# Kernel tuning notes

Measured on AMD Instinct MI355X. Metric: run time of the kernel, lower is better.

Reference implementation:

```python
import jax, jax.numpy as jnp
import numpy as np

H = 1024      # hidden_dim
C = 151       # len(obj_classes)
E = 200       # embed_dim (GloVe)
DIN = 2048    # inputs_dim
T = 32        # timesteps
B = 128       # batch size (uniform packed lengths)


def setup_inputs() -> dict:
    key = jax.random.key(0)
    ks = jax.random.split(key, 8)
    sequence_tensor = jax.random.normal(ks[0], (T * B, DIN), dtype=jnp.float32) * 0.1
    labels = jax.random.randint(ks[1], (T * B,), 0, C).astype(jnp.int64)
    embed = jax.random.normal(ks[2], (C + 1, E), dtype=jnp.float32) * 0.1   # obj_embed.weight
    Wi = jax.random.normal(ks[3], (DIN + E, 6 * H), dtype=jnp.float32) * 0.02  # input_linearity
    bi = jnp.zeros((6 * H,), dtype=jnp.float32)
    Ws = jax.random.normal(ks[4], (H, 5 * H), dtype=jnp.float32) * 0.02        # state_linearity
    bs = jnp.zeros((5 * H,), dtype=jnp.float32)
    Wo = jax.random.normal(ks[5], (H, C), dtype=jnp.float32) * 0.02            # out_obj
    bo = jnp.zeros((C,), dtype=jnp.float32)
    return {"sequence_tensor": sequence_tensor, "labels": labels, "embed": embed,
            "Wi": Wi, "bi": bi, "Ws": Ws, "bs": bs, "Wo": Wo, "bo": bo,
            "batch_size": B}


def reference(sequence_tensor, embed, Wi, bi, Ws, bs, Wo, bo, labels, batch_size):
    b = int(batch_size)
    t = sequence_tensor.shape[0] // b
    x = sequence_tensor.reshape(t, b, -1)          # [T, B, DIN] packed timestep-major
    lab = labels.reshape(t, b)                     # [T, B]
    h0 = jnp.zeros((b, H), dtype=sequence_tensor.dtype)
    c0 = jnp.zeros((b, H), dtype=sequence_tensor.dtype)
    e0 = jnp.broadcast_to(embed[0], (b, E))        # 'start' embedding

    def step(carry, inp):
        h, c, pe = carry
        xt, lt = inp
        ti = jnp.concatenate([xt, pe], axis=1)     # [B, DIN+E]
        pi = ti @ Wi + bi                          # [B, 6H]
        ps = h @ Ws + bs                           # [B, 5H]

        def gate(k):
            return pi[:, k * H:(k + 1) * H] + ps[:, k * H:(k + 1) * H]

        i_g = jax.nn.sigmoid(gate(0))
        f_g = jax.nn.sigmoid(gate(1))
        m_i = jnp.tanh(gate(2))
        o_g = jax.nn.sigmoid(gate(3))
        c_new = i_g * m_i + f_g * c
        out = o_g * jnp.tanh(c_new)
        hw = jax.nn.sigmoid(gate(4))
        h_new = hw * out + (1.0 - hw) * pi[:, 5 * H:6 * H]  # highway

        pred = h_new @ Wo + bo                     # [B, C]
        nzp = jnp.argmax(pred[:, 1:], axis=1) + 1  # best non-bg class
        l2e = jnp.where(lt == 0, nzp.astype(lt.dtype), lt)
        pe_new = embed[l2e + 1]                    # feedback embedding
        return (h_new, c_new, pe_new), (pred, l2e)

    _, (dists, comms) = jax.lax.scan(step, (h0, c0, e0), (x, lab))
    return dists.reshape(t * b, C), comms.reshape(t * b)
```

## Files before the change

### kernel.cpp

```cpp
#include <hip/hip_runtime.h>
#include <math.h>

#define H    1024
#define C    151
#define E    200
#define DIN  2048
#define T    32
#define B    128
#define SIXH  (6*H)
#define FIVEH (5*H)
#define KTOT  DIN
#define NEMB  (C+1)

typedef _Float16 f16x8 __attribute__((ext_vector_type(8)));
typedef _Float16 f16x4 __attribute__((ext_vector_type(4)));
typedef float    f32x4 __attribute__((ext_vector_type(4)));

#define GLOAD_LDS16(g, l) __builtin_amdgcn_global_load_lds( \
    (const __attribute__((address_space(1))) unsigned int*)(g), \
    (__attribute__((address_space(3))) unsigned int*)(l), 16, 0, 0)

__global__ void init_kernel(float* h, float* c, _Float16* hhi, _Float16* hlo, int* eidx) {
    int i = blockIdx.x * blockDim.x + threadIdx.x;
    if (i < B * H) {
        h[i] = 0.f; c[i] = 0.f;
        hhi[i] = (_Float16)0.f; hlo[i] = (_Float16)0.f;
    }
    if (i < B) eidx[i] = 0;
}

__global__ void cvt_x(const float* __restrict__ X, _Float16* __restrict__ hi,
                      _Float16* __restrict__ lo) {
    size_t i = ((size_t)blockIdx.x * 256 + threadIdx.x) * 4;
    float4 v = *(const float4*)(X + i);
    f16x4 h, l;
    h.x = (_Float16)v.x; l.x = (_Float16)(v.x - (float)h.x);
    h.y = (_Float16)v.y; l.y = (_Float16)(v.y - (float)h.y);
    h.z = (_Float16)v.z; l.z = (_Float16)(v.z - (float)h.z);
    h.w = (_Float16)v.w; l.w = (_Float16)(v.w - (float)h.w);
    *(f16x4*)(hi + i) = h;
    *(f16x4*)(lo + i) = l;
}

template<int KR, int NC>
__global__ void cvt_wT(const float* __restrict__ W, _Float16* __restrict__ hi,
                       _Float16* __restrict__ lo) {
    __shared__ float tile[32][33];
    int n0 = blockIdx.x * 32, k0 = blockIdx.y * 32;
    int tx = threadIdx.x & 31, ty = threadIdx.x >> 5;
    #pragma unroll
    for (int i = 0; i < 4; ++i) {
        int k = ty + i * 8;
        tile[k][tx] = W[(size_t)(k0 + k) * NC + n0 + tx];
    }
    __syncthreads();
    #pragma unroll
    for (int i = 0; i < 4; ++i) {
        int n = ty + i * 8;
        float v = tile[tx][n];
        _Float16 h = (_Float16)v;
        size_t o = (size_t)(n0 + n) * KR + k0 + tx;
        hi[o] = h;
        lo[o] = (_Float16)(v - (float)h);
    }
}

__global__ void etab_kernel(const float* __restrict__ embed,
                            const float* __restrict__ Wi,
                            float* __restrict__ Etab) {
    int n = blockIdx.x * 256 + threadIdx.x;
    int k = blockIdx.y;
    const float* wp = Wi + (size_t)DIN * SIXH + n;
    const float* ep = embed + k * E;
    float acc = 0.f;
    #pragma unroll 8
    for (int e = 0; e < E; ++e)
        acc = fmaf(ep[e], wp[(size_t)e * SIXH], acc);
    Etab[(size_t)k * SIXH + n] = acc;
}

__global__ __launch_bounds__(256) void big_gemm_mfma(
    const _Float16* __restrict__ Ahi, const _Float16* __restrict__ Alo,
    const _Float16* __restrict__ Bhi, const _Float16* __restrict__ Blo,
    const float* __restrict__ bi, float* __restrict__ P)
{
    __shared__ __align__(16) _Float16 sAh[128 * 32];
    __shared__ __align__(16) _Float16 sAl[128 * 32];
    __shared__ __align__(16) _Float16 sBh[128 * 32];
    __shared__ __align__(16) _Float16 sBl[128 * 32];
    const int tid = threadIdx.x;
    const int n0 = blockIdx.x * 128;
    const int m0 = blockIdx.y * 128;
    const int lane = tid & 63, w = tid >> 6;
    const int wm = (w >> 1) * 64, wn = (w & 1) * 64;
    const int lr = lane & 15, lq = lane >> 4;

    f32x4 acc[4][4];
    #pragma unroll
    for (int i = 0; i < 4; ++i)
        #pragma unroll
        for (int j = 0; j < 4; ++j)
            acc[i][j] = (f32x4){0.f, 0.f, 0.f, 0.f};

    const int row0 = tid >> 2;
    const int kc = tid & 3;

    for (int k0 = 0; k0 < KTOT; k0 += 32) {
        #pragma unroll
        for (int i = 0; i < 2; ++i) {
            int row = row0 + i * 64;
            size_t ga = (size_t)(m0 + row) * KTOT + k0 + kc * 8;
            size_t gb = (size_t)(n0 + row) * KTOT + k0 + kc * 8;
            int loff = (i * 256 + tid) * 8;
            GLOAD_LDS16(Ahi + ga, sAh + loff);
            GLOAD_LDS16(Alo + ga, sAl + loff);
            GLOAD_LDS16(Bhi + gb, sBh + loff);
            GLOAD_LDS16(Blo + gb, sBl + loff);
        }
        __syncthreads();
        f16x8 ah[4], al[4], bh[4], bl[4];
        #pragma unroll
        for (int i = 0; i < 4; ++i) {
            ah[i] = *(const f16x8*)&sAh[(wm + i * 16 + lr) * 32 + lq * 8];
            al[i] = *(const f16x8*)&sAl[(wm + i * 16 + lr) * 32 + lq * 8];
            bh[i] = *(const f16x8*)&sBh[(wn + i * 16 + lr) * 32 + lq * 8];
            bl[i] = *(const f16x8*)&sBl[(wn + i * 16 + lr) * 32 + lq * 8];
        }
        #pragma unroll
        for (int i = 0; i < 4; ++i)
            #pragma unroll
            for (int j = 0; j < 4; ++j) {
                acc[i][j] = __builtin_amdgcn_mfma_f32_16x16x32_f16(ah[i], bh[j], acc[i][j], 0, 0, 0);
                acc[i][j] = __builtin_amdgcn_mfma_f32_16x16x32_f16(ah[i], bl[j], acc[i][j], 0, 0, 0);
                acc[i][j] = __builtin_amdgcn_mfma_f32_16x16x32_f16(al[i], bh[j], acc[i][j], 0, 0, 0);
            }
        __syncthreads();
    }
    #pragma unroll
    for (int i = 0; i < 4; ++i)
        #pragma unroll
        for (int j = 0; j < 4; ++j) {
            int gcol = n0 + wn + j * 16 + lr;
            float bv = bi[gcol];
            #pragma unroll
            for (int r = 0; r < 4; ++r) {
                int grow = m0 + wm + i * 16 + lq * 4 + r;
                P[(size_t)grow * SIXH + gcol] = acc[i][j][r] + bv;
            }
        }
}

__global__ __launch_bounds__(256) void ps_mfma(
    const _Float16* __restrict__ Ahi, const _Float16* __restrict__ Alo,
    const _Float16* __restrict__ Bhi, const _Float16* __restrict__ Blo,
    float* __restrict__ ps)
{
    __shared__ __align__(16) _Float16 sAh[64 * 32];
    __shared__ __align__(16) _Float16 sAl[64 * 32];
    __shared__ __align__(16) _Float16 sBh[64 * 32];
    __shared__ __align__(16) _Float16 sBl[64 * 32];
    const int tid = threadIdx.x;
    const int n0 = blockIdx.x * 64;
    const int m0 = blockIdx.y * 64;
    const int lane = tid & 63, w = tid >> 6;
    const int wm = (w >> 1) * 32, wn = (w & 1) * 32;
    const int lr = lane & 15, lq = lane >> 4;

    f32x4 acc[2][2];
    #pragma unroll
    for (int i = 0; i < 2; ++i)
        #pragma unroll
        for (int j = 0; j < 2; ++j)
            acc[i][j] = (f32x4){0.f, 0.f, 0.f, 0.f};

    const int row = tid >> 2;
    const int kc = tid & 3;

    for (int k0 = 0; k0 < H; k0 += 32) {
        size_t ga = (size_t)(m0 + row) * H + k0 + kc * 8;
        size_t gb = (size_t)(n0 + row) * H + k0 + kc * 8;
        int loff = tid * 8;
        GLOAD_LDS16(Ahi + ga, sAh + loff);
        GLOAD_LDS16(Alo + ga, sAl + loff);
        GLOAD_LDS16(Bhi + gb, sBh + loff);
        GLOAD_LDS16(Blo + gb, sBl + loff);
        __syncthreads();
        f16x8 ah[2], al[2], bh[2], bl[2];
        #pragma unroll
        for (int i = 0; i < 2; ++i) {
            ah[i] = *(const f16x8*)&sAh[(wm + i * 16 + lr) * 32 + lq * 8];
            al[i] = *(const f16x8*)&sAl[(wm + i * 16 + lr) * 32 + lq * 8];
            bh[i] = *(const f16x8*)&sBh[(wn + i * 16 + lr) * 32 + lq * 8];
            bl[i] = *(const f16x8*)&sBl[(wn + i * 16 + lr) * 32 + lq * 8];
        }
        #pragma unroll
        for (int i = 0; i < 2; ++i)
            #pragma unroll
            for (int j = 0; j < 2; ++j) {
                acc[i][j] = __builtin_amdgcn_mfma_f32_16x16x32_f16(ah[i], bh[j], acc[i][j], 0, 0, 0);
                acc[i][j] = __builtin_amdgcn_mfma_f32_16x16x32_f16(ah[i], bl[j], acc[i][j], 0, 0, 0);
                acc[i][j] = __builtin_amdgcn_mfma_f32_16x16x32_f16(al[i], bh[j], acc[i][j], 0, 0, 0);
            }
        __syncthreads();
    }
    #pragma unroll
    for (int i = 0; i < 2; ++i)
        #pragma unroll
        for (int j = 0; j < 2; ++j) {
            int gcol = n0 + wn + j * 16 + lr;
            #pragma unroll
            for (int r = 0; r < 4; ++r) {
                int grow = m0 + wm + i * 16 + lq * 4 + r;
                ps[(size_t)grow * FIVEH + gcol] = acc[i][j][r];
            }
        }
}

__global__ void gate_kernel(const float* __restrict__ P,
                            const float* __restrict__ Etab,
                            const float* __restrict__ ps,
                            const float* __restrict__ bs,
                            const int* __restrict__ eidx,
                            float* __restrict__ h,
                            float* __restrict__ c,
                            _Float16* __restrict__ hhi,
                            _Float16* __restrict__ hlo,
                            int t) {
    int j = blockIdx.x * 256 + threadIdx.x;
    int b = blockIdx.y;
    const float* prow = P + (size_t)(t * B + b) * SIXH;
    const float* erow = Etab + (size_t)eidx[b] * SIXH;
    const float* psr  = ps + (size_t)b * FIVEH;
    float g[5];
    #pragma unroll
    for (int k = 0; k < 5; ++k) {
        int col = k * H + j;
        g[k] = prow[col] + erow[col] + psr[col] + bs[col];
    }
    float pi5 = prow[5 * H + j] + erow[5 * H + j];
    float ig = 1.f / (1.f + expf(-g[0]));
    float fg = 1.f / (1.f + expf(-g[1]));
    float mi = tanhf(g[2]);
    float og = 1.f / (1.f + expf(-g[3]));
    float hw = 1.f / (1.f + expf(-g[4]));
    float cv = c[b * H + j];
    float cn = ig * mi + fg * cv;
    float out = og * tanhf(cn);
    float hn = hw * out + (1.f - hw) * pi5;
    c[b * H + j] = cn;
    h[b * H + j] = hn;
    _Float16 hh = (_Float16)hn;
    hhi[b * H + j] = hh;
    hlo[b * H + j] = (_Float16)(hn - (float)hh);
}

__global__ void pred_kernel(const float* __restrict__ h,
                            const float* __restrict__ Wo,
                            const float* __restrict__ bo,
                            const int* __restrict__ labels,
                            float* __restrict__ dists,
                            float* __restrict__ comms,
                            int* __restrict__ eidx,
                            int t) {
    __shared__ float hs[H];
    __shared__ float vals[256];
    __shared__ int   idxs[256];
    int tid = threadIdx.x;
    int b = blockIdx.x;
    for (int i = tid; i < H / 4; i += 256)
        *(float4*)&hs[i * 4] = *(const float4*)&h[b * H + i * 4];
    __syncthreads();
    float pred = 0.f;
    if (tid < C) {
        pred = bo[tid];
        #pragma unroll 8
        for (int k = 0; k < H; ++k)
            pred = fmaf(hs[k], Wo[k * C + tid], pred);
        dists[(size_t)(t * B + b) * C + tid] = pred;
    }
    vals[tid] = (tid >= 1 && tid < C) ? pred : -1e30f;
    idxs[tid] = tid;
    __syncthreads();
    for (int s = 128; s > 0; s >>= 1) {
        if (tid < s) {
            float v2 = vals[tid + s];
            int   i2 = idxs[tid + s];
            if (v2 > vals[tid] || (v2 == vals[tid] && i2 < idxs[tid])) {
                vals[tid] = v2;
                idxs[tid] = i2;
            }
        }
        __syncthreads();
    }
    if (tid == 0) {
        int nzp = idxs[0];
        int lt = labels[t * B + b];
        int comm = (lt == 0) ? nzp : lt;
        comms[t * B + b] = (float)comm;
        eidx[b] = comm + 1;
    }
}

extern "C" void kernel_launch(void* const* d_in, const int* in_sizes, int n_in,
                              void* d_out, int out_size, void* d_ws, size_t ws_size,
                              hipStream_t stream) {
    const float* X      = (const float*)d_in[0];
    const int*   labels = (const int*)  d_in[1];
    const float* embed  = (const float*)d_in[2];
    const float* Wi     = (const float*)d_in[3];
    const float* bi     = (const float*)d_in[4];
    const float* Ws     = (const float*)d_in[5];
    const float* bs     = (const float*)d_in[6];
    const float* Wo     = (const float*)d_in[7];
    const float* bo     = (const float*)d_in[8];

    char* w = (char*)d_ws;
    float* P      = (float*)w;              w += (size_t)T * B * SIXH * 4;
    float* Etab   = (float*)w;              w += (size_t)NEMB * SIXH * 4;
    float* ps     = (float*)w;              w += (size_t)B * FIVEH * 4;
    float* h      = (float*)w;              w += (size_t)B * H * 4;
    float* c      = (float*)w;              w += (size_t)B * H * 4;
    _Float16* hhi = (_Float16*)w;           w += (size_t)B * H * 2;
    _Float16* hlo = (_Float16*)w;           w += (size_t)B * H * 2;
    int* eidx     = (int*)w;                w += 512;
    _Float16* Xhi = (_Float16*)w;           w += (size_t)T * B * KTOT * 2;
    _Float16* Xlo = (_Float16*)w;           w += (size_t)T * B * KTOT * 2;
    _Float16* WiThi = (_Float16*)w;         w += (size_t)SIXH * KTOT * 2;
    _Float16* WiTlo = (_Float16*)w;         w += (size_t)SIXH * KTOT * 2;
    _Float16* WsThi = (_Float16*)w;         w += (size_t)FIVEH * H * 2;
    _Float16* WsTlo = (_Float16*)w;         w += (size_t)FIVEH * H * 2;

    float* dists = (float*)d_out;
    float* comms = dists + (size_t)T * B * C;

    init_kernel<<<512, 256, 0, stream>>>(h, c, hhi, hlo, eidx);
    cvt_x<<<(T * B * KTOT) / (256 * 4), 256, 0, stream>>>(X, Xhi, Xlo);
    cvt_wT<KTOT, SIXH><<<dim3(SIXH / 32, KTOT / 32), 256, 0, stream>>>(Wi, WiThi, WiTlo);
    cvt_wT<H, FIVEH><<<dim3(FIVEH / 32, H / 32), 256, 0, stream>>>(Ws, WsThi, WsTlo);
    etab_kernel<<<dim3(SIXH / 256, NEMB), 256, 0, stream>>>(embed, Wi, Etab);
    big_gemm_mfma<<<dim3(SIXH / 128, (T * B) / 128), 256, 0, stream>>>(Xhi, Xlo, WiThi, WiTlo, bi, P);

    for (int t = 0; t < T; ++t) {
        ps_mfma<<<dim3(FIVEH / 64, B / 64), 256, 0, stream>>>(hhi, hlo, WsThi, WsTlo, ps);
        gate_kernel<<<dim3(H / 256, B), 256, 0, stream>>>(P, Etab, ps, bs, eidx, h, c, hhi, hlo, t);
        pred_kernel<<<B, 256, 0, stream>>>(h, Wo, bo, labels, dists, comms, eidx, t);
    }
}
```

Before: 2.561 ms.

## Run recurrent loop in one cooperative persistent kernel with fused gate and MFMA prediction

Replaces the per-timestep launches of the state GEMM, gate and prediction kernels with one cooperative persistent kernel. It has 128 blocks that compute the state GEMM split over K, fuse the gate math with the cell state kept in registers, and 8 blocks that compute the output projection with MFMA. Grid-wide syncs replace kernel boundaries, the prediction for step t-1 runs alongside the GEMM for step t, and the argmax becomes a wave shuffle reduction. The cost is two grid syncs per step and reliance on cooperative launch support, with a fused multi-launch fallback otherwise.

```diff
diff --git a/kernel.cpp b/kernel.cpp
--- a/kernel.cpp
+++ b/kernel.cpp
@@ -1,5 +1,8 @@
 #include <hip/hip_runtime.h>
+#include <hip/hip_cooperative_groups.h>
 #include <math.h>
+
+namespace cg = cooperative_groups;
 
 #define H    1024
 #define C    151
@@ -7,27 +10,21 @@
 #define DIN  2048
 #define T    32
 #define B    128
-#define SIXH  (6*H)
-#define FIVEH (5*H)
-#define KTOT  DIN
-#define NEMB  (C+1)
+#define SIXH  6144
+#define FIVEH 5120
+#define KTOT  2048
+#define NEMB  152
 
 typedef _Float16 f16x8 __attribute__((ext_vector_type(8)));
 typedef _Float16 f16x4 __attribute__((ext_vector_type(4)));
 typedef float    f32x4 __attribute__((ext_vector_type(4)));
 
+#define MFMA16(a, b, c) __builtin_amdgcn_mfma_f32_16x16x32_f16(a, b, c, 0, 0, 0)
 #define GLOAD_LDS16(g, l) __builtin_amdgcn_global_load_lds( \
     (const __attribute__((address_space(1))) unsigned int*)(g), \
     (__attribute__((address_space(3))) unsigned int*)(l), 16, 0, 0)
 
-__global__ void init_kernel(float* h, float* c, _Float16* hhi, _Float16* hlo, int* eidx) {
-    int i = blockIdx.x * blockDim.x + threadIdx.x;
-    if (i < B * H) {
-        h[i] = 0.f; c[i] = 0.f;
-        hhi[i] = (_Float16)0.f; hlo[i] = (_Float16)0.f;
-    }
-    if (i < B) eidx[i] = 0;
-}
+__device__ __forceinline__ float sigm(float x) { return 1.f / (1.f + expf(-x)); }
 
 __global__ void cvt_x(const float* __restrict__ X, _Float16* __restrict__ hi,
                       _Float16* __restrict__ lo) {
@@ -63,6 +60,16 @@
         hi[o] = h;
         lo[o] = (_Float16)(v - (float)h);
     }
+}
+
+__global__ void cvt_woT(const float* __restrict__ Wo, _Float16* __restrict__ hi,
+                        _Float16* __restrict__ lo) {
+    int idx = blockIdx.x * 256 + threadIdx.x;
+    int cc = idx >> 10, kk = idx & 1023;
+    float v = (cc < C) ? Wo[(size_t)kk * C + cc] : 0.f;
+    _Float16 h = (_Float16)v;
+    hi[idx] = h;
+    lo[idx] = (_Float16)(v - (float)h);
 }
 
 __global__ void etab_kernel(const float* __restrict__ embed,
@@ -130,9 +137,9 @@
         for (int i = 0; i < 4; ++i)
             #pragma unroll
             for (int j = 0; j < 4; ++j) {
-                acc[i][j] = __builtin_amdgcn_mfma_f32_16x16x32_f16(ah[i], bh[j], acc[i][j], 0, 0, 0);
-                acc[i][j] = __builtin_amdgcn_mfma_f32_16x16x32_f16(ah[i], bl[j], acc[i][j], 0, 0, 0);
-                acc[i][j] = __builtin_amdgcn_mfma_f32_16x16x32_f16(al[i], bh[j], acc[i][j], 0, 0, 0);
+                acc[i][j] = MFMA16(ah[i], bh[j], acc[i][j]);
+                acc[i][j] = MFMA16(ah[i], bl[j], acc[i][j]);
+                acc[i][j] = MFMA16(al[i], bh[j], acc[i][j]);
             }
         __syncthreads();
     }
@@ -150,155 +157,336 @@
         }
 }
 
-__global__ __launch_bounds__(256) void ps_mfma(
-    const _Float16* __restrict__ Ahi, const _Float16* __restrict__ Alo,
-    const _Float16* __restrict__ Bhi, const _Float16* __restrict__ Blo,
-    float* __restrict__ ps)
+__device__ __forceinline__ void pred_step(
+    int t, int m0,
+    const _Float16* __restrict__ hhi, const _Float16* __restrict__ hlo,
+    const _Float16* __restrict__ WoThi, const _Float16* __restrict__ WoTlo,
+    const float* __restrict__ bo, const int* __restrict__ labels,
+    float* __restrict__ dists, float* __restrict__ comms, int* __restrict__ eidx,
+    float (*smax)[10], int (*simax)[10])
 {
-    __shared__ __align__(16) _Float16 sAh[64 * 32];
-    __shared__ __align__(16) _Float16 sAl[64 * 32];
-    __shared__ __align__(16) _Float16 sBh[64 * 32];
-    __shared__ __align__(16) _Float16 sBl[64 * 32];
     const int tid = threadIdx.x;
-    const int n0 = blockIdx.x * 64;
-    const int m0 = blockIdx.y * 64;
     const int lane = tid & 63, w = tid >> 6;
-    const int wm = (w >> 1) * 32, wn = (w & 1) * 32;
     const int lr = lane & 15, lq = lane >> 4;
-
-    f32x4 acc[2][2];
+    #pragma unroll
+    for (int s = 0; s < 3; ++s) {
+        int nt = w + s * 4;
+        if (nt < 10) {
+            f32x4 p0 = (f32x4){0.f, 0.f, 0.f, 0.f};
+            f32x4 p1 = (f32x4){0.f, 0.f, 0.f, 0.f};
+            const _Float16* ha = hhi + (size_t)(m0 + lr) * H + lq * 8;
+            const _Float16* la = hlo + (size_t)(m0 + lr) * H + lq * 8;
+            const _Float16* hb = WoThi + (size_t)(nt * 16 + lr) * H + lq * 8;
+            const _Float16* lb = WoTlo + (size_t)(nt * 16 + lr) * H + lq * 8;
+            for (int k0 = 0; k0 < H; k0 += 64) {
+                f16x8 ah0 = *(const f16x8*)(ha + k0);
+                f16x8 al0 = *(const f16x8*)(la + k0);
+                f16x8 bh0 = *(const f16x8*)(hb + k0);
+                f16x8 bl0 = *(const f16x8*)(lb + k0);
+                f16x8 ah1 = *(const f16x8*)(ha + k0 + 32);
+                f16x8 al1 = *(const f16x8*)(la + k0 + 32);
+                f16x8 bh1 = *(const f16x8*)(hb + k0 + 32);
+                f16x8 bl1 = *(const f16x8*)(lb + k0 + 32);
+                p0 = MFMA16(ah0, bh0, p0); p0 = MFMA16(ah0, bl0, p0);
+                p0 = MFMA16(al0, bh0, p0); p0 = MFMA16(al0, bl0, p0);
+                p1 = MFMA16(ah1, bh1, p1); p1 = MFMA16(ah1, bl1, p1);
+                p1 = MFMA16(al1, bh1, p1); p1 = MFMA16(al1, bl1, p1);
+            }
+            int cls = nt * 16 + lr;
+            float bv = (cls < C) ? bo[cls] : 0.f;
+            float rv[4];
+            #pragma unroll
+            for (int r = 0; r < 4; ++r) {
+                float v = p0[r] + p1[r] + bv;
+                if (cls < C)
+                    dists[((size_t)t * B + m0 + lq * 4 + r) * C + cls] = v;
+                rv[r] = (cls >= 1 && cls < C) ? v : -3e38f;
+            }
+            #pragma unroll
+            for (int r = 0; r < 4; ++r) {
+                float mv = rv[r]; int mi = cls;
+                #pragma unroll
+                for (int m = 1; m <= 8; m <<= 1) {
+                    float ov = __shfl_xor(mv, m, 64);
+                    int   oi = __shfl_xor(mi, m, 64);
+                    if (ov > mv || (ov == mv && oi < mi)) { mv = ov; mi = oi; }
+                }
+                if (lr == 0) { smax[lq * 4 + r][nt] = mv; simax[lq * 4 + r][nt] = mi; }
+            }
+        }
+    }
+    __syncthreads();
+    if (tid < 16) {
+        float bv = -3e38f; int bx = 1 << 20;
+        #pragma unroll
+        for (int p = 0; p < 10; ++p) {
+            float v = smax[tid][p]; int ix = simax[tid][p];
+            if (v > bv || (v == bv && ix < bx)) { bv = v; bx = ix; }
+        }
+        int lt = labels[t * B + m0 + tid];
+        int cm = (lt == 0) ? bx : lt;
+        comms[(size_t)t * B + m0 + tid] = (float)cm;
+        eidx[m0 + tid] = cm + 1;
+    }
+    __syncthreads();
+}
+
+__global__ __launch_bounds__(256) void loop_coop(
+    const _Float16* __restrict__ WsThi, const _Float16* __restrict__ WsTlo,
+    const _Float16* __restrict__ WoThi, const _Float16* __restrict__ WoTlo,
+    const float* __restrict__ P, const float* __restrict__ Etab,
+    const float* __restrict__ bs, const float* __restrict__ bo,
+    const int* __restrict__ labels,
+    _Float16* __restrict__ hhi, _Float16* __restrict__ hlo,
+    float* __restrict__ psPart, int* __restrict__ eidx,
+    float* __restrict__ dists, float* __restrict__ comms)
+{
+    cg::grid_group grid = cg::this_grid();
+    const int bid = blockIdx.x;
+    const int tid = threadIdx.x;
+    const int lane = tid & 63, w = tid >> 6;
+    const int lr = lane & 15, lq = lane >> 4;
+
+    __shared__ __align__(16) _Float16 sAh[128 * 32];
+    __shared__ __align__(16) _Float16 sAl[128 * 32];
+    __shared__ __align__(16) _Float16 sBh[80 * 32];
+    __shared__ __align__(16) _Float16 sBl[80 * 32];
+    __shared__ float smax[16][10];
+    __shared__ int   simax[16][10];
+
+    const bool isG = bid < 128;
+    const int nt = bid >> 1, kh = bid & 1;
+    const int n0 = nt * 16;
+    const int m0p = (bid - 128) * 16;
+
+    float c_reg[2][4] = {{0.f,0.f,0.f,0.f},{0.f,0.f,0.f,0.f}};
+
+    for (int k = 0; k <= T; ++k) {
+        f32x4 acc[2][5];
+        #pragma unroll
+        for (int i = 0; i < 2; ++i)
+            #pragma unroll
+            for (int g = 0; g < 5; ++g)
+                acc[i][g] = (f32x4){0.f, 0.f, 0.f, 0.f};
+
+        if (isG) {
+            if (k >= 1 && k < T) {
+                const int kbase = kh * 512;
+                for (int k0 = 0; k0 < 512; k0 += 32) {
+                    #pragma unroll
+                    for (int ii = 0; ii < 2; ++ii) {
+                        int s = ii * 256 + tid;
+                        int row = s >> 2, kc = s & 3;
+                        size_t ga = (size_t)row * H + kbase + k0 + kc * 8;
+                        GLOAD_LDS16(hhi + ga, sAh + s * 8);
+                        GLOAD_LDS16(hlo + ga, sAl + s * 8);
+                    }
+                    {
+                        int s = tid;
+                        int brow = s >> 2, kc = s & 3;
+                        size_t gb = (size_t)((brow >> 4) * H + n0 + (brow & 15)) * H
+                                    + kbase + k0 + kc * 8;
+                        GLOAD_LDS16(WsThi + gb, sBh + s * 8);
+                        GLOAD_LDS16(WsTlo + gb, sBl + s * 8);
+                    }
+                    if (tid < 64) {
+                        int s = 256 + tid;
+                        int brow = s >> 2, kc = s & 3;
+                        size_t gb = (size_t)((brow >> 4) * H + n0 + (brow & 15)) * H
+                                    + kbase + k0 + kc * 8;
+                        GLOAD_LDS16(WsThi + gb, sBh + s * 8);
+                        GLOAD_LDS16(WsTlo + gb, sBl + s * 8);
+                    }
+                    __syncthreads();
+                    f16x8 ah[2], al[2];
+                    #pragma unroll
+                    for (int i = 0; i < 2; ++i) {
+                        ah[i] = *(const f16x8*)&sAh[((w * 2 + i) * 16 + lr) * 32 + lq * 8];
+                        al[i] = *(const f16x8*)&sAl[((w * 2 + i) * 16 + lr) * 32 + lq * 8];
+                    }
+                    #pragma unroll
+                    for (int g = 0; g < 5; ++g) {
+                        f16x8 bh = *(const f16x8*)&sBh[(g * 16 + lr) * 32 + lq * 8];
+                        f16x8 bl = *(const f16x8*)&sBl[(g * 16 + lr) * 32 + lq * 8];
+                        #pragma unroll
+                        for (int i = 0; i < 2; ++i) {
+                            acc[i][g] = MFMA16(ah[i], bh, acc[i][g]);
+                            acc[i][g] = MFMA16(ah[i], bl, acc[i][g]);
+                            acc[i][g] = MFMA16(al[i], bh, acc[i][g]);
+                        }
+                    }
+                    __syncthreads();
+                }
+                if (kh == 1) {
+                    #pragma unroll
+                    for (int i = 0; i < 2; ++i)
+                        #pragma unroll
+                        for (int g = 0; g < 5; ++g)
+                            #pragma unroll
+                            for (int r = 0; r < 4; ++r) {
+                                int bb = (w * 2 + i) * 16 + lq * 4 + r;
+                                psPart[((size_t)nt * 128 + bb) * 80 + g * 16 + lr] = acc[i][g][r];
+                            }
+                }
+            }
+        } else {
+            if (k >= 1)
+                pred_step(k - 1, m0p, hhi, hlo, WoThi, WoTlo, bo, labels,
+                          dists, comms, eidx, smax, simax);
+        }
+        grid.sync();
+
+        if (isG && kh == 0 && k < T) {
+            #pragma unroll
+            for (int i = 0; i < 2; ++i)
+                #pragma unroll
+                for (int r = 0; r < 4; ++r) {
+                    int bb = (w * 2 + i) * 16 + lq * 4 + r;
+                    int j = n0 + lr;
+                    int e = (k >= 1) ? eidx[bb] : 0;
+                    size_t pbase  = ((size_t)k * B + bb) * SIXH + j;
+                    size_t ebase  = (size_t)e * SIXH + j;
+                    size_t ppbase = ((size_t)nt * 128 + bb) * 80 + lr;
+                    float gv[5];
+                    #pragma unroll
+                    for (int g = 0; g < 5; ++g) {
+                        float part = (k >= 1) ? psPart[ppbase + g * 16] : 0.f;
+                        gv[g] = acc[i][g][r] + part + P[pbase + g * 1024]
+                                + Etab[ebase + g * 1024] + bs[g * 1024 + j];
+                    }
+                    float p5 = P[pbase + 5 * 1024] + Etab[ebase + 5 * 1024];
+                    float ig  = sigm(gv[0]);
+                    float fg  = sigm(gv[1]);
+                    float mi_ = tanhf(gv[2]);
+                    float og  = sigm(gv[3]);
+                    float hw  = sigm(gv[4]);
+                    float cn  = ig * mi_ + fg * c_reg[i][r];
+                    float out = og * tanhf(cn);
+                    float hn  = hw * out + (1.f - hw) * p5;
+                    c_reg[i][r] = cn;
+                    _Float16 hh = (_Float16)hn;
+                    hhi[(size_t)bb * H + j] = hh;
+                    hlo[(size_t)bb * H + j] = (_Float16)(hn - (float)hh);
+                }
+        }
+        if (k < T) grid.sync();
+    }
+}
+
+__global__ __launch_bounds__(256) void psgate_kernel(
+    const _Float16* __restrict__ hPhi, const _Float16* __restrict__ hPlo,
+    _Float16* __restrict__ hOhi, _Float16* __restrict__ hOlo,
+    const _Float16* __restrict__ WsThi, const _Float16* __restrict__ WsTlo,
+    const float* __restrict__ P, const float* __restrict__ Etab,
+    const float* __restrict__ bs, const int* __restrict__ eidx,
+    float* __restrict__ c, int t)
+{
+    const int tid = threadIdx.x;
+    const int lane = tid & 63, w = tid >> 6;
+    const int lr = lane & 15, lq = lane >> 4;
+    const int nt = blockIdx.x;
+    const int n0 = nt * 16;
+
+    __shared__ __align__(16) _Float16 sAh[128 * 32];
+    __shared__ __align__(16) _Float16 sAl[128 * 32];
+    __shared__ __align__(16) _Float16 sBh[80 * 32];
+    __shared__ __align__(16) _Float16 sBl[80 * 32];
+
+    f32x4 acc[2][5];
     #pragma unroll
     for (int i = 0; i < 2; ++i)
         #pragma unroll
-        for (int j = 0; j < 2; ++j)
-            acc[i][j] = (f32x4){0.f, 0.f, 0.f, 0.f};
-
-    const int row = tid >> 2;
-    const int kc = tid & 3;
-
-    for (int k0 = 0; k0 < H; k0 += 32) {
-        size_t ga = (size_t)(m0 + row) * H + k0 + kc * 8;
-        size_t gb = (size_t)(n0 + row) * H + k0 + kc * 8;
-        int loff = tid * 8;
-        GLOAD_LDS16(Ahi + ga, sAh + loff);
-        GLOAD_LDS16(Alo + ga, sAl + loff);
-        GLOAD_LDS16(Bhi + gb, sBh + loff);
-        GLOAD_LDS16(Blo + gb, sBl + loff);
-        __syncthreads();
-        f16x8 ah[2], al[2], bh[2], bl[2];
-        #pragma unroll
-        for (int i = 0; i < 2; ++i) {
-            ah[i] = *(const f16x8*)&sAh[(wm + i * 16 + lr) * 32 + lq * 8];
-            al[i] = *(const f16x8*)&sAl[(wm + i * 16 + lr) * 32 + lq * 8];
-            bh[i] = *(const f16x8*)&sBh[(wn + i * 16 + lr) * 32 + lq * 8];
-            bl[i] = *(const f16x8*)&sBl[(wn + i * 16 + lr) * 32 + lq * 8];
-        }
-        #pragma unroll
-        for (int i = 0; i < 2; ++i)
-            #pragma unroll
-            for (int j = 0; j < 2; ++j) {
-                acc[i][j] = __builtin_amdgcn_mfma_f32_16x16x32_f16(ah[i], bh[j], acc[i][j], 0, 0, 0);
-                acc[i][j] = __builtin_amdgcn_mfma_f32_16x16x32_f16(ah[i], bl[j], acc[i][j], 0, 0, 0);
-                acc[i][j] = __builtin_amdgcn_mfma_f32_16x16x32_f16(al[i], bh[j], acc[i][j], 0, 0, 0);
-            }
-        __syncthreads();
-    }
+        for (int g = 0; g < 5; ++g)
+            acc[i][g] = (f32x4){0.f, 0.f, 0.f, 0.f};
+
+    if (t > 0) {
+        for (int k0 = 0; k0 < H; k0 += 32) {
+            #pragma unroll
+            for (int ii = 0; ii < 2; ++ii) {
+                int s = ii * 256 + tid;
+                int row = s >> 2, kc = s & 3;
+                size_t ga = (size_t)row * H + k0 + kc * 8;
+                GLOAD_LDS16(hPhi + ga, sAh + s * 8);
+                GLOAD_LDS16(hPlo + ga, sAl + s * 8);
+            }
+            {
+                int s = tid;
+                int brow = s >> 2, kc = s & 3;
+                size_t gb = (size_t)((brow >> 4) * H + n0 + (brow & 15)) * H + k0 + kc * 8;
+                GLOAD_LDS16(WsThi + gb, sBh + s * 8);
+                GLOAD_LDS16(WsTlo + gb, sBl + s * 8);
+            }
+            if (tid < 64) {
+                int s = 256 + tid;
+                int brow = s >> 2, kc = s & 3;
+                size_t gb = (size_t)((brow >> 4) * H + n0 + (brow & 15)) * H + k0 + kc * 8;
+                GLOAD_LDS16(WsThi + gb, sBh + s * 8);
+                GLOAD_LDS16(WsTlo + gb, sBl + s * 8);
+            }
+            __syncthreads();
+            f16x8 ah[2], al[2];
+            #pragma unroll
+            for (int i = 0; i < 2; ++i) {
+                ah[i] = *(const f16x8*)&sAh[((w * 2 + i) * 16 + lr) * 32 + lq * 8];
+                al[i] = *(const f16x8*)&sAl[((w * 2 + i) * 16 + lr) * 32 + lq * 8];
+            }
+            #pragma unroll
+            for (int g = 0; g < 5; ++g) {
+                f16x8 bh = *(const f16x8*)&sBh[(g * 16 + lr) * 32 + lq * 8];
+                f16x8 bl = *(const f16x8*)&sBl[(g * 16 + lr) * 32 + lq * 8];
+                #pragma unroll
+                for (int i = 0; i < 2; ++i) {
+                    acc[i][g] = MFMA16(ah[i], bh, acc[i][g]);
+                    acc[i][g] = MFMA16(ah[i], bl, acc[i][g]);
+                    acc[i][g] = MFMA16(al[i], bh, acc[i][g]);
+                }
+            }
+            __syncthreads();
+        }
+    }
+
     #pragma unroll
     for (int i = 0; i < 2; ++i)
         #pragma unroll
-        for (int j = 0; j < 2; ++j) {
-            int gcol = n0 + wn + j * 16 + lr;
-            #pragma unroll
-            for (int r = 0; r < 4; ++r) {
-                int grow = m0 + wm + i * 16 + lq * 4 + r;
-                ps[(size_t)grow * FIVEH + gcol] = acc[i][j][r];
-            }
-        }
-}
-
-__global__ void gate_kernel(const float* __restrict__ P,
-                            const float* __restrict__ Etab,
-                            const float* __restrict__ ps,
-                            const float* __restrict__ bs,
-                            const int* __restrict__ eidx,
-                            float* __restrict__ h,
-                            float* __restrict__ c,
-                            _Float16* __restrict__ hhi,
-                            _Float16* __restrict__ hlo,
-                            int t) {
-    int j = blockIdx.x * 256 + threadIdx.x;
-    int b = blockIdx.y;
-    const float* prow = P + (size_t)(t * B + b) * SIXH;
-    const float* erow = Etab + (size_t)eidx[b] * SIXH;
-    const float* psr  = ps + (size_t)b * FIVEH;
-    float g[5];
-    #pragma unroll
-    for (int k = 0; k < 5; ++k) {
-        int col = k * H + j;
-        g[k] = prow[col] + erow[col] + psr[col] + bs[col];
-    }
-    float pi5 = prow[5 * H + j] + erow[5 * H + j];
-    float ig = 1.f / (1.f + expf(-g[0]));
-    float fg = 1.f / (1.f + expf(-g[1]));
-    float mi = tanhf(g[2]);
-    float og = 1.f / (1.f + expf(-g[3]));
-    float hw = 1.f / (1.f + expf(-g[4]));
-    float cv = c[b * H + j];
-    float cn = ig * mi + fg * cv;
-    float out = og * tanhf(cn);
-    float hn = hw * out + (1.f - hw) * pi5;
-    c[b * H + j] = cn;
-    h[b * H + j] = hn;
-    _Float16 hh = (_Float16)hn;
-    hhi[b * H + j] = hh;
-    hlo[b * H + j] = (_Float16)(hn - (float)hh);
-}
-
-__global__ void pred_kernel(const float* __restrict__ h,
-                            const float* __restrict__ Wo,
-                            const float* __restrict__ bo,
-                            const int* __restrict__ labels,
-                            float* __restrict__ dists,
-                            float* __restrict__ comms,
-                            int* __restrict__ eidx,
-                            int t) {
-    __shared__ float hs[H];
-    __shared__ float vals[256];
-    __shared__ int   idxs[256];
-    int tid = threadIdx.x;
-    int b = blockIdx.x;
-    for (int i = tid; i < H / 4; i += 256)
-        *(float4*)&hs[i * 4] = *(const float4*)&h[b * H + i * 4];
-    __syncthreads();
-    float pred = 0.f;
-    if (tid < C) {
-        pred = bo[tid];
-        #pragma unroll 8
-        for (int k = 0; k < H; ++k)
-            pred = fmaf(hs[k], Wo[k * C + tid], pred);
-        dists[(size_t)(t * B + b) * C + tid] = pred;
-    }
-    vals[tid] = (tid >= 1 && tid < C) ? pred : -1e30f;
-    idxs[tid] = tid;
-    __syncthreads();
-    for (int s = 128; s > 0; s >>= 1) {
-        if (tid < s) {
-            float v2 = vals[tid + s];
-            int   i2 = idxs[tid + s];
-            if (v2 > vals[tid] || (v2 == vals[tid] && i2 < idxs[tid])) {
-                vals[tid] = v2;
-                idxs[tid] = i2;
-            }
-        }
-        __syncthreads();
-    }
-    if (tid == 0) {
-        int nzp = idxs[0];
-        int lt = labels[t * B + b];
-        int comm = (lt == 0) ? nzp : lt;
-        comms[t * B + b] = (float)comm;
-        eidx[b] = comm + 1;
-    }
+        for (int r = 0; r < 4; ++r) {
+            int bb = (w * 2 + i) * 16 + lq * 4 + r;
+            int j = n0 + lr;
+            int e = (t > 0) ? eidx[bb] : 0;
+            size_t pbase = ((size_t)t * B + bb) * SIXH + j;
+            size_t ebase = (size_t)e * SIXH + j;
+            float gv[5];
+            #pragma unroll
+            for (int g = 0; g < 5; ++g)
+                gv[g] = acc[i][g][r] + P[pbase + g * 1024]
+                        + Etab[ebase + g * 1024] + bs[g * 1024 + j];
+            float p5 = P[pbase + 5 * 1024] + Etab[ebase + 5 * 1024];
+            float ig  = sigm(gv[0]);
+            float fg  = sigm(gv[1]);
+            float mi_ = tanhf(gv[2]);
+            float og  = sigm(gv[3]);
+            float hw  = sigm(gv[4]);
+            float cv  = (t > 0) ? c[(size_t)bb * H + j] : 0.f;
+            float cn  = ig * mi_ + fg * cv;
+            float out = og * tanhf(cn);
+            float hn  = hw * out + (1.f - hw) * p5;
+            c[(size_t)bb * H + j] = cn;
+            _Float16 hh = (_Float16)hn;
+            hOhi[(size_t)bb * H + j] = hh;
+            hOlo[(size_t)bb * H + j] = (_Float16)(hn - (float)hh);
+        }
+}
+
+__global__ __launch_bounds__(256) void pred_kernel8(
+    const _Float16* __restrict__ hhi, const _Float16* __restrict__ hlo,
+    const _Float16* __restrict__ WoThi, const _Float16* __restrict__ WoTlo,
+    const float* __restrict__ bo, const int* __restrict__ labels,
+    float* __restrict__ dists, float* __restrict__ comms,
+    int* __restrict__ eidx, int t)
+{
+    __shared__ float smax[16][10];
+    __shared__ int   simax[16][10];
+    pred_step(t, blockIdx.x * 16, hhi, hlo, WoThi, WoTlo, bo, labels,
+              dists, comms, eidx, smax, simax);
 }
 
 extern "C" void kernel_launch(void* const* d_in, const int* in_sizes, int n_in,
@@ -315,34 +503,65 @@
     const float* bo     = (const float*)d_in[8];
 
     char* w = (char*)d_ws;
-    float* P      = (float*)w;              w += (size_t)T * B * SIXH * 4;
-    float* Etab   = (float*)w;              w += (size_t)NEMB * SIXH * 4;
-    float* ps     = (float*)w;              w += (size_t)B * FIVEH * 4;
-    float* h      = (float*)w;              w += (size_t)B * H * 4;
-    float* c      = (float*)w;              w += (size_t)B * H * 4;
-    _Float16* hhi = (_Float16*)w;           w += (size_t)B * H * 2;
-    _Float16* hlo = (_Float16*)w;           w += (size_t)B * H * 2;
-    int* eidx     = (int*)w;                w += 512;
-    _Float16* Xhi = (_Float16*)w;           w += (size_t)T * B * KTOT * 2;
-    _Float16* Xlo = (_Float16*)w;           w += (size_t)T * B * KTOT * 2;
-    _Float16* WiThi = (_Float16*)w;         w += (size_t)SIXH * KTOT * 2;
-    _Float16* WiTlo = (_Float16*)w;         w += (size_t)SIXH * KTOT * 2;
-    _Float16* WsThi = (_Float16*)w;         w += (size_t)FIVEH * H * 2;
-    _Float16* WsTlo = (_Float16*)w;         w += (size_t)FIVEH * H * 2;
+    float* P        = (float*)w;    w += (size_t)T * B * SIXH * 4;
+    float* Etab     = (float*)w;    w += (size_t)NEMB * SIXH * 4;
+    _Float16* Xhi   = (_Float16*)w; w += (size_t)T * B * KTOT * 2;
+    _Float16* Xlo   = (_Float16*)w; w += (size_t)T * B * KTOT * 2;
+    char* overlay   = w;
+    _Float16* WiThi = (_Float16*)w; w += (size_t)SIXH * KTOT * 2;
+    _Float16* WiTlo = (_Float16*)w; w += (size_t)SIXH * KTOT * 2;
+
+    char* r = overlay;
+    _Float16* WsThi = (_Float16*)r; r += (size_t)FIVEH * H * 2;
+    _Float16* WsTlo = (_Float16*)r; r += (size_t)FIVEH * H * 2;
+    _Float16* WoThi = (_Float16*)r; r += (size_t)160 * H * 2;
+    _Float16* WoTlo = (_Float16*)r; r += (size_t)160 * H * 2;
+    _Float16* hhiA  = (_Float16*)r; r += (size_t)B * H * 2;
+    _Float16* hloA  = (_Float16*)r; r += (size_t)B * H * 2;
+    _Float16* hhiB  = (_Float16*)r; r += (size_t)B * H * 2;
+    _Float16* hloB  = (_Float16*)r; r += (size_t)B * H * 2;
+    float* cArr     = (float*)r;    r += (size_t)B * H * 4;
+    float* psPart   = (float*)r;    r += (size_t)64 * 128 * 80 * 4;
+    int*   eidx     = (int*)r;      r += 512;
 
     float* dists = (float*)d_out;
     float* comms = dists + (size_t)T * B * C;
 
-    init_kernel<<<512, 256, 0, stream>>>(h, c, hhi, hlo, eidx);
     cvt_x<<<(T * B * KTOT) / (256 * 4), 256, 0, stream>>>(X, Xhi, Xlo);
     cvt_wT<KTOT, SIXH><<<dim3(SIXH / 32, KTOT / 32), 256, 0, stream>>>(Wi, WiThi, WiTlo);
-    cvt_wT<H, FIVEH><<<dim3(FIVEH / 32, H / 32), 256, 0, stream>>>(Ws, WsThi, WsTlo);
     etab_kernel<<<dim3(SIXH / 256, NEMB), 256, 0, stream>>>(embed, Wi, Etab);
     big_gemm_mfma<<<dim3(SIXH / 128, (T * B) / 128), 256, 0, stream>>>(Xhi, Xlo, WiThi, WiTlo, bi, P);
-
-    for (int t = 0; t < T; ++t) {
-        ps_mfma<<<dim3(FIVEH / 64, B / 64), 256, 0, stream>>>(hhi, hlo, WsThi, WsTlo, ps);
-        gate_kernel<<<dim3(H / 256, B), 256, 0, stream>>>(P, Etab, ps, bs, eidx, h, c, hhi, hlo, t);
-        pred_kernel<<<B, 256, 0, stream>>>(h, Wo, bo, labels, dists, comms, eidx, t);
-    }
-}
+    cvt_wT<H, FIVEH><<<dim3(FIVEH / 32, H / 32), 256, 0, stream>>>(Ws, WsThi, WsTlo);
+    cvt_woT<<<(160 * H) / 256, 256, 0, stream>>>(Wo, WoThi, WoTlo);
+
+    bool launched = false;
+    int dev = 0;
+    if (hipGetDevice(&dev) == hipSuccess) {
+        int coopAttr = 0, numCU = 0, occ = 0;
+        hipDeviceGetAttribute(&coopAttr, hipDeviceAttributeCooperativeLaunch, dev);
+        hipDeviceGetAttribute(&numCU, hipDeviceAttributeMultiprocessorCount, dev);
+        hipOccupancyMaxActiveBlocksPerMultiprocessor(&occ, (const void*)loop_coop, 256, 0);
+        if (coopAttr && (long)occ * numCU >= 136) {
+            void* args[] = {
+                (void*)&WsThi, (void*)&WsTlo, (void*)&WoThi, (void*)&WoTlo,
+                (void*)&P, (void*)&Etab, (void*)&bs, (void*)&bo, (void*)&labels,
+                (void*)&hhiA, (void*)&hloA, (void*)&psPart, (void*)&eidx,
+                (void*)&dists, (void*)&comms
+            };
+            launched = hipLaunchCooperativeKernel((void*)loop_coop, dim3(136), dim3(256),
+                                                  args, 0, stream) == hipSuccess;
+        }
+    }
+    if (!launched) {
+        for (int t = 0; t < T; ++t) {
+            _Float16* rdHi = (t & 1) ? hhiA : hhiB;
+            _Float16* rdLo = (t & 1) ? hloA : hloB;
+            _Float16* wrHi = (t & 1) ? hhiB : hhiA;
+            _Float16* wrLo = (t & 1) ? hloB : hloA;
+            psgate_kernel<<<64, 256, 0, stream>>>(rdHi, rdLo, wrHi, wrLo,
+                                                  WsThi, WsTlo, P, Etab, bs, eidx, cArr, t);
+            pred_kernel8<<<8, 256, 0, stream>>>(wrHi, wrLo, WoThi, WoTlo, bo, labels,
+                                                dists, comms, eidx, t);
+        }
+    }
+}
```

New measurement: 3.128 ms. 22.2% more time.
